# Kernel optimization log

Hardware: AMD Instinct MI355X
Metric: run time of the kernel (lower is better)

The kernel has to match this reference:

```python
import jax, jax.numpy as jnp
import numpy as np

B, H, W, C = 4, 48, 48, 768
L = H * W
D_STATE, D_CONV, D_INNER = 16, 4, C  # expand=1
DT_RANK = (C + 15) // 16  # 48


def generate_cross_scan_indices(Hh, Ww):
    indices = []
    visited = set()
    ch, cw = Hh // 2, Ww // 2
    indices.append((ch, cw)); visited.add((ch, cw))
    for radius in range(1, max(Hh, Ww)):
        for r in range(1, radius + 1):
            p = (ch - r, cw)
            if 0 <= p[0] < Hh and 0 <= p[1] < Ww and p not in visited: indices.append(p); visited.add(p)
        for r in range(1, radius + 1):
            p = (ch, cw + r)
            if 0 <= p[0] < Hh and 0 <= p[1] < Ww and p not in visited: indices.append(p); visited.add(p)
        for r in range(1, radius + 1):
            p = (ch + r, cw)
            if 0 <= p[0] < Hh and 0 <= p[1] < Ww and p not in visited: indices.append(p); visited.add(p)
        for r in range(1, radius + 1):
            p = (ch, cw - r)
            if 0 <= p[0] < Hh and 0 <= p[1] < Ww and p not in visited: indices.append(p); visited.add(p)
        for r in range(1, radius + 1):
            for p in [(ch - r, cw + r), (ch + r, cw + r), (ch + r, cw - r), (ch - r, cw - r)]:
                if 0 <= p[0] < Hh and 0 <= p[1] < Ww and p not in visited: indices.append(p); visited.add(p)
        for i in range(-radius, radius + 1):
            for j in range(-radius, radius + 1):
                p = (ch + i, cw + j)
                if 0 <= p[0] < Hh and 0 <= p[1] < Ww and p not in visited: indices.append(p); visited.add(p)
    return np.array([i * Ww + j for i, j in indices], dtype=np.int32)


def _mamba_params(key, scale=0.02):
    ks = jax.random.split(key, 6)
    return dict(
        in_w=jax.random.normal(ks[0], (2 * D_INNER, C)) * scale,
        conv_w=jax.random.normal(ks[1], (D_INNER, 1, D_CONV)) * scale,
        conv_b=jnp.zeros((D_INNER,)),
        xproj_w=jax.random.normal(ks[2], (DT_RANK + 2 * D_STATE, D_INNER)) * scale,
        dt_w=jax.random.normal(ks[3], (D_INNER, DT_RANK)) * scale,
        dt_b=jax.random.normal(ks[4], (D_INNER,)) * 0.1,
        A_log=jnp.broadcast_to(jnp.log(jnp.arange(1, D_STATE + 1, dtype=jnp.float32)), (D_INNER, D_STATE)).copy(),
        Dp=jnp.ones((D_INNER,)),
        out_w=jax.random.normal(ks[5], (C, D_INNER)) * scale,
    )


def setup_inputs() -> dict:
    key = jax.random.key(0)
    kx, kf, kb, k1, k2 = jax.random.split(key, 5)
    fp = _mamba_params(kf)
    bp = _mamba_params(kb)
    inp = {
        'x': jax.random.normal(kx, (B, L, C), dtype=jnp.float32),
        'scan_idx': jnp.asarray(generate_cross_scan_indices(H, W)),
        'norm_g': jnp.ones((C,)), 'norm_b': jnp.zeros((C,)),
        'fuse_w1': jax.random.normal(k1, (C, 2 * C)) * 0.02, 'fuse_b1': jnp.zeros((C,)),
        'fuse_w2': jax.random.normal(k2, (C, C)) * 0.02, 'fuse_b2': jnp.zeros((C,)),
    }
    for pre, p in (('f_', fp), ('b_', bp)):
        for n, v in p.items():
            inp[pre + n] = v
    return inp


def silu(v):
    return v * jax.nn.sigmoid(v)


def mamba(x, in_w, conv_w, conv_b, xproj_w, dt_w, dt_b, A_log, Dp, out_w):
    Bn, Ln, _ = x.shape
    xz = x @ in_w.T                      # [B,L,2*d_inner]
    xi, z = jnp.split(xz, 2, axis=-1)
    # causal depthwise conv1d, kernel D_CONV, left pad D_CONV-1
    xp = jnp.pad(xi, ((0, 0), (D_CONV - 1, 0), (0, 0)))
    xc = sum(conv_w[:, 0, k] * xp[:, k:k + Ln, :] for k in range(D_CONV)) + conv_b
    xc = silu(xc)                        # [B,L,d_inner]
    x_dbl = xc @ xproj_w.T
    dt, Bm, Cm = jnp.split(x_dbl, [DT_RANK, DT_RANK + D_STATE], axis=-1)
    dt = jax.nn.softplus(dt @ dt_w.T + dt_b)  # [B,L,d_inner]
    A = -jnp.exp(A_log)                  # [d_inner,d_state]

    def step(h, inps):
        dt_t, B_t, C_t, x_t = inps       # [B,d],[B,s],[B,s],[B,d]
        dA = jnp.exp(dt_t[:, :, None] * A)
        h = dA * h + (dt_t * x_t)[:, :, None] * B_t[:, None, :]
        y = jnp.einsum('bds,bs->bd', h, C_t)
        return h, y

    h0 = jnp.zeros((Bn, D_INNER, D_STATE), xc.dtype)
    xs = (dt.transpose(1, 0, 2), Bm.transpose(1, 0, 2), Cm.transpose(1, 0, 2), xc.transpose(1, 0, 2))
    _, ys = jax.lax.scan(step, h0, xs)
    y = ys.transpose(1, 0, 2) + Dp * xc
    y = y * silu(z)
    return y @ out_w.T


def reference(x, scan_idx, norm_g, norm_b, fuse_w1, fuse_b1, fuse_w2, fuse_b2,
              f_in_w, f_conv_w, f_conv_b, f_xproj_w, f_dt_w, f_dt_b, f_A_log, f_Dp, f_out_w,
              b_in_w, b_conv_w, b_conv_b, b_xproj_w, b_dt_w, b_dt_b, b_A_log, b_Dp, b_out_w):
    residual = x
    mu = x.mean(-1, keepdims=True)
    var = ((x - mu) ** 2).mean(-1, keepdims=True)
    xn = (x - mu) / jnp.sqrt(var + 1e-6) * norm_g + norm_b
    rev = jnp.argsort(scan_idx)
    xf = mamba(xn[:, scan_idx, :], f_in_w, f_conv_w, f_conv_b, f_xproj_w, f_dt_w, f_dt_b, f_A_log, f_Dp, f_out_w)[:, rev, :]
    flip = scan_idx[::-1]
    xb = mamba(xn[:, flip, :], b_in_w, b_conv_w, b_conv_b, b_xproj_w, b_dt_w, b_dt_b, b_A_log, b_Dp, b_out_w)[:, jnp.argsort(flip), :]
    fused = jnp.concatenate([xf, xb], axis=-1)
    h = jax.nn.gelu(fused @ fuse_w1.T + fuse_b1, approximate=False)
    out = h @ fuse_w2.T + fuse_b2
    return out + residual
```

## Files before the change

### kernel.cpp

```cpp
#include <hip/hip_runtime.h>
#include <hip/hip_bf16.h>
#include <cmath>

#define BB 4
#define LL 2304
#define CC 768
#define DSTATE 16
#define DINNER 768
#define DTRANK 48
#define MTOK (BB*LL)
#define NCH 48
#define LCH (LL/NCH)

#define S_XZ   14155776L
#define S_XC   7077888L
#define S_DT   7077888L
#define S_BC   294912L
#define S_YB   7077888L
#define S_AP   2359296L

#define L2E 1.4426950408889634f

typedef __bf16 bf16_t;
typedef __bf16 bf16x8 __attribute__((ext_vector_type(8)));
typedef float  f32x4  __attribute__((ext_vector_type(4)));

__device__ __forceinline__ float silu_f(float v){ return v / (1.0f + __expf(-v)); }
__device__ __forceinline__ float softplus_f(float v){
    return fmaxf(v,0.f) + __logf(1.0f + __expf(-fabsf(v)));
}

typedef __attribute__((address_space(3))) void  lds_vt;
typedef __attribute__((address_space(1))) void  gbl_vt;
__device__ __forceinline__ void async_copy16(const void* g, void* l){
    __builtin_amdgcn_global_load_lds((const gbl_vt*)g, (lds_vt*)l, 16, 0, 0);
}

__global__ __launch_bounds__(256)
void wconv_k(const float* __restrict__ a0, const float* __restrict__ a1,
             const float* __restrict__ a2, const float* __restrict__ a3,
             const float* __restrict__ a4, const float* __restrict__ a5,
             bf16_t* __restrict__ dst)
{
    const int cum[7]  = {0,1179648,2359296,3538944,4128768,4153344,4177920};
    const int dofs[6] = {0,1179648,2359296,3538944,4718592,5332992};
    const float* srcs[6] = {a0,a1,a2,a3,a4,a5};
    int idx = blockIdx.x*256 + threadIdx.x;
    if (idx >= 4177920) return;
    int seg = 0;
    while (idx >= cum[seg+1]) ++seg;
    dst[dofs[seg] + idx - cum[seg]] = (bf16_t)srcs[seg][idx - cum[seg]];
}

__global__ __launch_bounds__(256)
void transp_k(const float* __restrict__ s0, const float* __restrict__ s1,
              bf16_t* __restrict__ d0, bf16_t* __restrict__ d1)
{
    __shared__ float tile[32][33];
    const float* src = blockIdx.z ? s1 : s0;
    bf16_t* dst = blockIdx.z ? d1 : d0;
    int c0 = blockIdx.y*32, d0c = blockIdx.x*32;
    int tx = threadIdx.x & 31, ty = threadIdx.x >> 5;
#pragma unroll
    for (int r=0;r<4;++r)
        tile[ty+8*r][tx] = src[(long)(c0+ty+8*r)*768 + d0c+tx];
    __syncthreads();
#pragma unroll
    for (int r=0;r<4;++r)
        dst[(long)(d0c+ty+8*r)*768 + c0+tx] = (bf16_t)tile[tx][ty+8*r];
}

__global__ __launch_bounds__(256)
void inv_k(const int* __restrict__ sidx, int* __restrict__ rf, int* __restrict__ rb)
{
    int t = blockIdx.x*256 + threadIdx.x;
    if (t >= LL) return;
    rf[sidx[t]] = t;
    rb[sidx[LL-1-t]] = t;
}

__global__ __launch_bounds__(256)
void combo_k(const float* __restrict__ dtw, const float* __restrict__ xproj,
             bf16_t* __restrict__ dst)
{
    __shared__ float row[48];
    int n = blockIdx.x;
    if (threadIdx.x < 48) row[threadIdx.x] = dtw[n*48 + threadIdx.x];
    __syncthreads();
#pragma unroll
    for (int kk=0; kk<3; ++kk){
        int k = threadIdx.x + 256*kk;
        float s = 0.f;
#pragma unroll 8
        for (int r=0; r<48; ++r) s += row[r]*xproj[r*768 + k];
        dst[n*768 + k] = (bf16_t)s;
    }
}

__global__ __launch_bounds__(256)
void ln_k(const float* __restrict__ x, const float* __restrict__ g,
          const float* __restrict__ bta, bf16_t* __restrict__ xn)
{
    int row = blockIdx.x;
    const float* xr = x + (long)row*CC;
    int tid = threadIdx.x;
    float v[3];
#pragma unroll
    for (int r=0;r<3;++r) v[r] = xr[tid + 256*r];
    float s  = v[0]+v[1]+v[2];
    float s2 = v[0]*v[0]+v[1]*v[1]+v[2]*v[2];
    __shared__ float red[8];
    for (int o=32;o;o>>=1){ s += __shfl_down(s,o); s2 += __shfl_down(s2,o); }
    int wv = tid>>6, ln = tid&63;
    if (ln==0){ red[wv]=s; red[4+wv]=s2; }
    __syncthreads();
    if (tid==0){
        red[0] = red[0]+red[1]+red[2]+red[3];
        red[4] = red[4]+red[5]+red[6]+red[7];
    }
    __syncthreads();
    float mu  = red[0]*(1.0f/CC);
    float var = red[4]*(1.0f/CC) - mu*mu;
    float rstd = rsqrtf(var + 1e-6f);
#pragma unroll
    for (int r=0;r<3;++r){
        int c = tid + 256*r;
        xn[(long)row*CC + c] = (bf16_t)((v[r]-mu)*rstd*g[c] + bta[c]);
    }
}

#define CT 8
__global__ __launch_bounds__(256)
void conv_k(const bf16_t* __restrict__ xz, const float* __restrict__ cw0,
            const float* __restrict__ cw1, const float* __restrict__ cb0,
            const float* __restrict__ cb1, bf16_t* __restrict__ xc)
{
    int dir = blockIdx.y;
    const bf16_t* xzd = xz + (long)dir*S_XZ;
    const float* cw = dir ? cw1 : cw0;
    const float* cb = dir ? cb1 : cb0;
    bf16_t* xcd = xc + (long)dir*S_XC;
    int idx = blockIdx.x*256 + threadIdx.x;
    if (idx >= (MTOK/CT)*(DINNER/8)) return;
    int dg    = idx % (DINNER/8);
    int chunk = idx / (DINNER/8);
    int d0 = dg*8;
    long r0 = (long)chunk*CT;
    int t0 = (int)(r0 % LL);

    float4 wv[8];
#pragma unroll
    for (int u=0;u<8;++u) wv[u] = *(const float4*)&cw[(d0+u)*4];
    float bz[8];
#pragma unroll
    for (int u=0;u<8;++u) bz[u] = cb[d0+u];

    const bf16_t* src = xzd + r0*1536 + d0;
    bf16x8 win0, win1, win2;
    if (t0 >= 3){
        win0 = *(const bf16x8*)(src - 3*1536);
        win1 = *(const bf16x8*)(src - 2*1536);
        win2 = *(const bf16x8*)(src - 1*1536);
    } else {
#pragma unroll
        for (int u=0;u<8;++u){ win0[u]=(bf16_t)0.f; win1[u]=(bf16_t)0.f; win2[u]=(bf16_t)0.f; }
    }
#pragma unroll
    for (int t=0;t<CT;++t){
        bf16x8 cur = *(const bf16x8*)(src + (long)t*1536);
        bf16x8 o;
#pragma unroll
        for (int u=0;u<8;++u){
            float acc = bz[u]
                + wv[u].x*(float)win0[u] + wv[u].y*(float)win1[u]
                + wv[u].z*(float)win2[u] + wv[u].w*(float)cur[u];
            o[u] = (bf16_t)silu_f(acc);
        }
        *(bf16x8*)(xcd + (r0+t)*DINNER + d0) = o;
        win0 = win1; win1 = win2; win2 = cur;
    }
}

template<int GATHER, int SCATTER, int EPI>
__global__ __launch_bounds__(256)
void gemm4_k(const bf16_t* __restrict__ A, long a_stride, int lda,
             const bf16_t* __restrict__ W0, const bf16_t* __restrict__ W1,
             int N, int K,
             void* __restrict__ out1, long o1_stride,
             void* __restrict__ out2, long o2_stride,
             int ldc, int ccol_stride,
             const float* __restrict__ bias0, const float* __restrict__ bias1,
             const float* __restrict__ resid,
             const int* __restrict__ sidx,
             const int* __restrict__ ridx0, const int* __restrict__ ridx1)
{
    __shared__ __align__(16) bf16_t smem[2*128*64];
    bf16_t* As = smem;
    bf16_t* Bs = smem + 128*64;

    const int tid  = threadIdx.x;
    const int lane = tid & 63;
    const int w    = tid >> 6;
    const int ln16 = lane & 15;
    const int q    = lane >> 4;
    const int dir  = blockIdx.z;

    const bf16_t* Ad = A + (long)dir*a_stride;
    const bf16_t* W  = dir ? W1 : W0;
    const float* bias = dir ? bias1 : bias0;

    const int m0 = blockIdx.x*128;
    const int n0 = blockIdx.y*128;

    const int srow = lane >> 3;
    const int csrc = (lane & 7) ^ srow;
    const bf16_t* gA[4]; const bf16_t* gA1[4]; const bf16_t* gB[4];
#pragma unroll
    for (int inst=0; inst<4; ++inst){
        int row = w*32 + inst*8 + srow;
        int r = m0 + row;
        if (GATHER == 4){
            int t = r % LL; int bo = r - t;
            gA[inst]  = A + (long)(bo + ridx0[t])*lda + csrc*8;
            gA1[inst] = A + a_stride + (long)(bo + ridx1[t])*lda + csrc*8;
        } else {
            int sr = r;
            if (GATHER == 3){
                int t = r % LL; int bo = r - t;
                sr = bo + (dir ? sidx[LL-1-t] : sidx[t]);
            }
            gA[inst] = Ad + (long)sr*lda + csrc*8;
        }
        int n = n0 + row; if (n >= N) n = N-1;
        gB[inst] = W + (long)n*K + csrc*8;
    }

    f32x4 acc[4][4];
#pragma unroll
    for (int i=0;i<4;++i)
#pragma unroll
      for (int j=0;j<4;++j) acc[i][j] = (f32x4){0.f,0.f,0.f,0.f};

    const int e = ln16 & 7;
    const int ar_base = ((w>>1)*64 + ln16)*64;
    const int br_base = ((w&1)*64 + ln16)*64;

    for (int k0 = 0; k0 < K; k0 += 64){
#pragma unroll
        for (int inst=0; inst<4; ++inst){
            bf16_t* la = As + (w*256 + inst*64)*8;
            bf16_t* lb = Bs + (w*256 + inst*64)*8;
            const bf16_t* asrc;
            if (GATHER == 4)
                asrc = (k0 >= 768) ? (gA1[inst] + (k0 - 768)) : (gA[inst] + k0);
            else
                asrc = gA[inst] + k0;
            async_copy16(asrc, la);
            async_copy16(gB[inst] + k0, lb);
        }
        __syncthreads();
#pragma unroll
        for (int kk=0; kk<2; ++kk){
            const int ce = (((kk<<2)|q) ^ e)*8;
            bf16x8 af[4], bf[4];
#pragma unroll
            for (int i=0;i<4;++i) af[i] = *(const bf16x8*)&As[ar_base + i*16*64 + ce];
#pragma unroll
            for (int j=0;j<4;++j) bf[j] = *(const bf16x8*)&Bs[br_base + j*16*64 + ce];
#pragma unroll
            for (int i=0;i<4;++i)
#pragma unroll
              for (int j=0;j<4;++j)
                acc[i][j] = __builtin_amdgcn_mfma_f32_16x16x32_bf16(af[i], bf[j], acc[i][j], 0,0,0);
        }
        __syncthreads();
    }

    const int mw = (w>>1)*64;
    const int nw = (w&1)*64;
    const int ccolb = ccol_stride*dir;

    const bool staged = (EPI==2) || (EPI==3) || (EPI==5 && n0 < 768);
    if (staged){
        bf16_t* Cs = smem;
#pragma unroll
        for (int i=0;i<4;++i){
#pragma unroll
            for (int reg=0; reg<4; ++reg){
                int rowl = mw + i*16 + q*4 + reg;
#pragma unroll
                for (int j=0;j<4;++j){
                    int coll = nw + j*16 + ln16;
                    float v = acc[i][j][reg];
                    if (EPI==3){
                        v += bias[n0 + coll];
                        v = 0.5f*v*(1.0f + erff(v*0.70710678118654752f));
                    } else if (EPI==5){
                        v = softplus_f(v + bias[n0 + coll]);
                    }
                    Cs[rowl*128 + coll] = (bf16_t)v;
                }
            }
        }
        __syncthreads();
        bf16_t* o = (bf16_t*)out1 + (long)dir*o1_stride;
#pragma unroll
        for (int c=0;c<8;++c){
            int chunk = tid + 256*c;
            int rowl = chunk >> 4;
            int coll = (chunk & 15)*8;
            int r = m0 + rowl;
            int orow = r;
            if (SCATTER == 3){
                int t = r % LL; int bo = r - t;
                orow = bo + (dir ? sidx[LL-1-t] : sidx[t]);
            }
            *(int4*)&o[(long)orow*ldc + ccolb + n0 + coll] = *(const int4*)&Cs[rowl*128 + coll];
        }
    } else {
#pragma unroll
        for (int i=0;i<4;++i){
#pragma unroll
            for (int reg=0; reg<4; ++reg){
                int r = m0 + mw + i*16 + q*4 + reg;
#pragma unroll
                for (int j=0;j<4;++j){
                    int col = n0 + nw + j*16 + ln16;
                    if (col >= N) continue;
                    float v = acc[i][j][reg];
                    if (EPI==4){
                        v += bias[col] + resid[(long)r*CC + col];
                        ((float*)out1)[(long)r*ldc + col] = v;
                    } else {
                        ((float*)out2 + (long)dir*o2_stride)[(long)r*32 + (col-768)] = v;
                    }
                }
            }
        }
    }
}

template<int PASS>
__global__ __launch_bounds__(256)
void scanp_k(const bf16_t* __restrict__ dtp, const bf16_t* __restrict__ xcp,
             const float* __restrict__ bcp, const bf16_t* __restrict__ xzp,
             const float* __restrict__ Al0, const float* __restrict__ Al1,
             const float* __restrict__ Dp0, const float* __restrict__ Dp1,
             float* __restrict__ Aprod, float* __restrict__ Hend,
             bf16_t* __restrict__ yout)
{
    __shared__ __align__(16) float s_bc[LCH*32];

    const int dir = blockIdx.y;
    int blk = blockIdx.x;
    const int dblk = blk % 3; int tmp = blk / 3;
    const int j = tmp % NCH; const int b = tmp / NCH;
    const int tid = threadIdx.x;
    const long tbase = (long)b*LL + (long)j*LCH;
    const int d = dblk*256 + tid;

    const float* gbc = bcp + dir*S_BC + tbase*32;
    async_copy16(gbc + tid*4, s_bc + tid*4);
    if (tid < 128) async_copy16(gbc + (256+tid)*4, s_bc + (256+tid)*4);

    const float* Al = dir ? Al1 : Al0;
    float ac2[16]; bool fast = true;
#pragma unroll
    for (int k=0;k<16;++k){
        float a = -__expf(Al[d*DSTATE + k]);
        fast = fast && (fabsf(a + (float)(k+1)) < 1e-3f*(float)(k+1));
        ac2[k] = a * L2E;
    }

    __syncthreads();

    const bf16_t* gdt = dtp + dir*S_DT + tbase*DINNER + d;
    const bf16_t* gxc = xcp + dir*S_XC + tbase*DINNER + d;
    const bf16_t* gz  = xzp + dir*S_XZ + tbase*1536 + DINNER + d;
    bf16_t* gy = yout + dir*S_YB + tbase*DINNER + d;

    const long o = dir*S_AP + ((long)(b*NCH + j)*DINNER + d)*DSTATE;

    float h[16];
    float dpv = 0.f;
    if (PASS==3){
#pragma unroll
        for (int g=0; g<4; ++g){
            f32x4 hv = *(const f32x4*)&Aprod[o + 4*g];
#pragma unroll
            for (int k=0;k<4;++k) h[g*4+k] = hv[k];
        }
        dpv = (dir ? Dp1 : Dp0)[d];
    } else {
#pragma unroll
        for (int k=0;k<16;++k) h[k] = 0.f;
    }
    float sdt = 0.f;

#pragma unroll 2
    for (int t=0; t<LCH; ++t){
        float dt = (float)gdt[(long)t*DINNER];
        float xv = (float)gxc[(long)t*DINNER];
        float ek[16];
        if (fast){
            float e1 = __builtin_amdgcn_exp2f(-L2E*dt);
            ek[0]=e1;        ek[1]=e1*e1;      ek[2]=ek[1]*e1;   ek[3]=ek[1]*ek[1];
            ek[4]=ek[3]*e1;  ek[5]=ek[3]*ek[1];ek[6]=ek[3]*ek[2];ek[7]=ek[3]*ek[3];
            ek[8]=ek[7]*e1;  ek[9]=ek[7]*ek[1];ek[10]=ek[7]*ek[2];ek[11]=ek[7]*ek[3];
            ek[12]=ek[7]*ek[4];ek[13]=ek[7]*ek[5];ek[14]=ek[7]*ek[6];ek[15]=ek[7]*ek[7];
        } else {
#pragma unroll
            for (int k=0;k<16;++k) ek[k] = __builtin_amdgcn_exp2f(dt*ac2[k]);
        }
        float c = dt*xv;
        if (PASS==1) sdt += dt;
        const float* bcr = &s_bc[t*32];
#pragma unroll
        for (int g=0; g<4; ++g){
            f32x4 Bv = *(const f32x4*)&bcr[g*4];
#pragma unroll
            for (int k=0;k<4;++k) h[g*4+k] = ek[g*4+k]*h[g*4+k] + c*Bv[k];
        }
        if (PASS==3){
            f32x4 Cv0 = *(const f32x4*)&bcr[16];
            f32x4 Cv1 = *(const f32x4*)&bcr[20];
            f32x4 Cv2 = *(const f32x4*)&bcr[24];
            f32x4 Cv3 = *(const f32x4*)&bcr[28];
            float p0=0.f,p1=0.f,p2=0.f,p3=0.f;
#pragma unroll
            for (int k=0;k<4;++k){
                p0 += h[k]*Cv0[k];    p1 += h[4+k]*Cv1[k];
                p2 += h[8+k]*Cv2[k];  p3 += h[12+k]*Cv3[k];
            }
            float p = (p0+p1)+(p2+p3);
            float zv = (float)gz[(long)t*1536];
            gy[(long)t*DINNER] = (bf16_t)((p + dpv*xv) * silu_f(zv));
        }
    }

    if (PASS==1){
        float ap[16];
        if (fast){
            float e1 = __builtin_amdgcn_exp2f(-L2E*sdt);
            ap[0]=e1;        ap[1]=e1*e1;      ap[2]=ap[1]*e1;   ap[3]=ap[1]*ap[1];
            ap[4]=ap[3]*e1;  ap[5]=ap[3]*ap[1];ap[6]=ap[3]*ap[2];ap[7]=ap[3]*ap[3];
            ap[8]=ap[7]*e1;  ap[9]=ap[7]*ap[1];ap[10]=ap[7]*ap[2];ap[11]=ap[7]*ap[3];
            ap[12]=ap[7]*ap[4];ap[13]=ap[7]*ap[5];ap[14]=ap[7]*ap[6];ap[15]=ap[7]*ap[7];
        } else {
#pragma unroll
            for (int k=0;k<16;++k) ap[k] = __builtin_amdgcn_exp2f(sdt*ac2[k]);
        }
#pragma unroll
        for (int g=0; g<4; ++g){
            f32x4 av, hv;
#pragma unroll
            for (int k=0;k<4;++k){ av[k]=ap[g*4+k]; hv[k]=h[g*4+k]; }
            *(f32x4*)&Aprod[o+4*g] = av;
            *(f32x4*)&Hend[o+4*g]  = hv;
        }
    }
}

__global__ __launch_bounds__(256)
void scan2_k(float* __restrict__ Aprod, const float* __restrict__ Hend)
{
    int idx = blockIdx.x*256 + threadIdx.x;
    if (idx >= 2*BB*DINNER*DSTATE) return;
    int dir = idx / (BB*DINNER*DSTATE);
    int rem = idx - dir*(BB*DINNER*DSTATE);
    int b = rem / (DINNER*DSTATE);
    int ds = rem % (DINNER*DSTATE);
    long base = (long)dir*S_AP;
    float h = 0.f;
    for (int j=0;j<NCH;++j){
        long o = base + (long)(b*NCH+j)*DINNER*DSTATE + ds;
        float ap = Aprod[o];
        float he = Hend[o];
        Aprod[o] = h;
        h = ap*h + he;
    }
}

extern "C" void kernel_launch(void* const* d_in, const int* in_sizes, int n_in,
                              void* d_out, int out_size, void* d_ws, size_t ws_size,
                              hipStream_t stream)
{
    const float* x       = (const float*)d_in[0];
    const int*   sidx    = (const int*)  d_in[1];
    const float* norm_g  = (const float*)d_in[2];
    const float* norm_b  = (const float*)d_in[3];
    const float* fuse_w1 = (const float*)d_in[4];
    const float* fuse_b1 = (const float*)d_in[5];
    const float* fuse_w2 = (const float*)d_in[6];
    const float* fuse_b2 = (const float*)d_in[7];
    const float* f_in_w   = (const float*)d_in[8];
    const float* f_conv_w = (const float*)d_in[9];
    const float* f_conv_b = (const float*)d_in[10];
    const float* f_xproj  = (const float*)d_in[11];
    const float* f_dt_w   = (const float*)d_in[12];
    const float* f_dt_b   = (const float*)d_in[13];
    const float* f_A_log  = (const float*)d_in[14];
    const float* f_Dp     = (const float*)d_in[15];
    const float* f_out_w  = (const float*)d_in[16];
    const float* b_in_w   = (const float*)d_in[17];
    const float* b_conv_w = (const float*)d_in[18];
    const float* b_conv_b = (const float*)d_in[19];
    const float* b_xproj  = (const float*)d_in[20];
    const float* b_dt_w   = (const float*)d_in[21];
    const float* b_dt_b   = (const float*)d_in[22];
    const float* b_A_log  = (const float*)d_in[23];
    const float* b_Dp     = (const float*)d_in[24];
    const float* b_out_w  = (const float*)d_in[25];
    float* out = (float*)d_out;

    float* ws    = (float*)d_ws;
    bf16_t* xn   = (bf16_t*)ws;
    bf16_t* xz   = (bf16_t*)(ws + 3538944);
    bf16_t* xc   = (bf16_t*)(ws + 17694720);
    bf16_t* dtb  = (bf16_t*)(ws + 24772608);
    float* bc    = ws + 31850496;
    bf16_t* yb   = (bf16_t*)(ws + 32440320);
    bf16_t* h1   = (bf16_t*)(ws + 39518208);
    float* Aprod = ws + 43057152;
    float* Hend  = ws + 47775744;
    bf16_t* wbf  = (bf16_t*)(ws + 52494336);
    int* rev_f   = (int*)(ws + 56352768);
    int* rev_b   = rev_f + 2304;

    bf16_t* w_fin    = wbf + 0;
    bf16_t* w_bin    = wbf + 1179648;
    bf16_t* w_1      = wbf + 2359296;
    bf16_t* w_2      = wbf + 3538944;
    bf16_t* w_fcombo = wbf + 4128768;
    bf16_t* w_bcombo = wbf + 4743168;
    bf16_t* foutT    = wbf + 5357568;
    bf16_t* boutT    = wbf + 5947392;
    bf16_t* Ccat     = wbf + 6537216;

    wconv_k<<<16320, 256, 0, stream>>>(f_in_w, b_in_w, fuse_w1, fuse_w2,
                                       f_xproj + 48*768, b_xproj + 48*768, wbf);
    transp_k<<<dim3(24,24,2), 256, 0, stream>>>(f_out_w, b_out_w, foutT, boutT);
    inv_k<<<9, 256, 0, stream>>>(sidx, rev_f, rev_b);
    combo_k<<<768, 256, 0, stream>>>(f_dt_w, f_xproj, w_fcombo);
    combo_k<<<768, 256, 0, stream>>>(b_dt_w, b_xproj, w_bcombo);
    ln_k<<<MTOK, 256, 0, stream>>>(x, norm_g, norm_b, xn);
    gemm4_k<0,0,2><<<dim3(6,6,2), 256, 0, stream>>>(
        w_1, 768, 1536, foutT, boutT, 768, 768,
        Ccat, 0, nullptr, 0, 1536, 768, nullptr, nullptr, nullptr, nullptr,
        nullptr, nullptr);

    gemm4_k<3,0,2><<<dim3(72,12,2), 256, 0, stream>>>(
        xn, 0, CC, w_fin, w_bin, 1536, 768,
        xz, S_XZ, nullptr, 0, 1536, 0, nullptr, nullptr, nullptr, sidx,
        nullptr, nullptr);
    conv_k<<<dim3((MTOK/CT)*(DINNER/8)/256, 2), 256, 0, stream>>>(
        xz, f_conv_w, b_conv_w, f_conv_b, b_conv_b, xc);
    gemm4_k<0,0,5><<<dim3(72,7,2), 256, 0, stream>>>(
        xc, S_XC, DINNER, w_fcombo, w_bcombo, 800, 768,
        dtb, S_DT, bc, S_BC, 768, 0, f_dt_b, b_dt_b, nullptr, nullptr,
        nullptr, nullptr);
    scanp_k<1><<<dim3(BB*NCH*3,2), 256, 0, stream>>>(
        dtb, xc, bc, xz, f_A_log, b_A_log, f_Dp, b_Dp, Aprod, Hend, yb);
    scan2_k<<<384, 256, 0, stream>>>(Aprod, Hend);
    scanp_k<3><<<dim3(BB*NCH*3,2), 256, 0, stream>>>(
        dtb, xc, bc, xz, f_A_log, b_A_log, f_Dp, b_Dp, Aprod, Hend, yb);
    gemm4_k<4,0,3><<<dim3(72,6,1), 256, 0, stream>>>(
        yb, S_YB, DINNER, Ccat, Ccat, 768, 1536,
        h1, 0, nullptr, 0, 768, 0, fuse_b1, fuse_b1, nullptr, nullptr,
        rev_f, rev_b);
    gemm4_k<0,0,4><<<dim3(72,6,1), 256, 0, stream>>>(
        h1, 0, DINNER, w_2, w_2, 768, 768,
        out, 0, nullptr, 0, 768, 0, fuse_b2, fuse_b2, x, nullptr,
        nullptr, nullptr);
}
```

Measured before the change: 505.8 us.

## Store xz, xc and dt in time-packed layout for vectorized scan loads

The in-projection and dt/B/C GEMMs now write their outputs in a layout where 8 consecutive timesteps of each channel are contiguous. The scan kernel can then fetch dt, x and z as 16-byte vectors once every 8 steps instead of strided scalar loads every step. The conv kernel reads this packed layout and writes both a packed copy for the scan and a row-major copy for the next GEMM, reusing the xn and h1 buffers. The cost is extra transposing work in the GEMM epilogues and a second conv output write, plus reliance on those aliased buffers being free at that point.

```diff
diff --git a/kernel.cpp b/kernel.cpp
--- a/kernel.cpp
+++ b/kernel.cpp
@@ -18,6 +18,7 @@
 #define S_BC   294912L
 #define S_YB   7077888L
 #define S_AP   2359296L
+#define S_XCR  79036416L
 
 #define L2E 1.4426950408889634f
 
@@ -35,6 +36,7 @@
 __device__ __forceinline__ void async_copy16(const void* g, void* l){
     __builtin_amdgcn_global_load_lds((const gbl_vt*)g, (lds_vt*)l, 16, 0, 0);
 }
+
 
 __global__ __launch_bounds__(256)
 void wconv_k(const float* __restrict__ a0, const float* __restrict__ a1,
@@ -129,55 +131,53 @@
     }
 }
 
-#define CT 8
-__global__ __launch_bounds__(256)
-void conv_k(const bf16_t* __restrict__ xz, const float* __restrict__ cw0,
+__global__ __launch_bounds__(256)
+void conv_k(const bf16_t* __restrict__ xzT, const float* __restrict__ cw0,
             const float* __restrict__ cw1, const float* __restrict__ cb0,
-            const float* __restrict__ cb1, bf16_t* __restrict__ xc)
-{
-    int dir = blockIdx.y;
-    const bf16_t* xzd = xz + (long)dir*S_XZ;
+            const float* __restrict__ cb1, bf16_t* __restrict__ xcT,
+            bf16_t* __restrict__ xcR0, bf16_t* __restrict__ xcR1)
+{
+    const int dir = blockIdx.y;
+    const bf16_t* src = xzT + (long)dir*S_XZ;
+    bf16_t* dstT = xcT + (long)dir*S_XC;
+    bf16_t* dstR = dir ? xcR1 : xcR0;
     const float* cw = dir ? cw1 : cw0;
     const float* cb = dir ? cb1 : cb0;
-    bf16_t* xcd = xc + (long)dir*S_XC;
     int idx = blockIdx.x*256 + threadIdx.x;
-    if (idx >= (MTOK/CT)*(DINNER/8)) return;
-    int dg    = idx % (DINNER/8);
-    int chunk = idx / (DINNER/8);
-    int d0 = dg*8;
-    long r0 = (long)chunk*CT;
-    int t0 = (int)(r0 % LL);
-
-    float4 wv[8];
-#pragma unroll
-    for (int u=0;u<8;++u) wv[u] = *(const float4*)&cw[(d0+u)*4];
-    float bz[8];
-#pragma unroll
-    for (int u=0;u<8;++u) bz[u] = cb[d0+u];
-
-    const bf16_t* src = xzd + r0*1536 + d0;
-    bf16x8 win0, win1, win2;
-    if (t0 >= 3){
-        win0 = *(const bf16x8*)(src - 3*1536);
-        win1 = *(const bf16x8*)(src - 2*1536);
-        win2 = *(const bf16x8*)(src - 1*1536);
-    } else {
-#pragma unroll
-        for (int u=0;u<8;++u){ win0[u]=(bf16_t)0.f; win1[u]=(bf16_t)0.f; win2[u]=(bf16_t)0.f; }
-    }
-#pragma unroll
-    for (int t=0;t<CT;++t){
-        bf16x8 cur = *(const bf16x8*)(src + (long)t*1536);
-        bf16x8 o;
-#pragma unroll
-        for (int u=0;u<8;++u){
-            float acc = bz[u]
-                + wv[u].x*(float)win0[u] + wv[u].y*(float)win1[u]
-                + wv[u].z*(float)win2[u] + wv[u].w*(float)cur[u];
-            o[u] = (bf16_t)silu_f(acc);
-        }
-        *(bf16x8*)(xcd + (r0+t)*DINNER + d0) = o;
-        win0 = win1; win1 = win2; win2 = cur;
+    int d = idx % 768;
+    int chunk = idx / 768;
+    int tb = chunk*2;
+    int r0 = chunk*16;
+
+    bf16x8 c0 = *(const bf16x8*)&src[((long)tb*1536 + d)*8];
+    bf16x8 c1 = *(const bf16x8*)&src[((long)(tb+1)*1536 + d)*8];
+    float xm3, xm2, xm1;
+    if (r0 % LL){
+        bf16x8 pv = *(const bf16x8*)&src[((long)(tb-1)*1536 + d)*8];
+        xm3=(float)pv[5]; xm2=(float)pv[6]; xm1=(float)pv[7];
+    } else { xm3=0.f; xm2=0.f; xm1=0.f; }
+
+    float4 w = *(const float4*)&cw[d*4];
+    float bz = cb[d];
+
+    float xx[16];
+#pragma unroll
+    for (int u=0;u<8;++u){ xx[u]=(float)c0[u]; xx[8+u]=(float)c1[u]; }
+    bf16x8 o0, o1;
+#pragma unroll
+    for (int u=0;u<16;++u){
+        float cur = xx[u];
+        float acc = bz + w.x*xm3 + w.y*xm2 + w.z*xm1 + w.w*cur;
+        float r = silu_f(acc);
+        if (u < 8) o0[u] = (bf16_t)r; else o1[u-8] = (bf16_t)r;
+        xm3 = xm2; xm2 = xm1; xm1 = cur;
+    }
+    *(bf16x8*)&dstT[((long)tb*768 + d)*8]     = o0;
+    *(bf16x8*)&dstT[((long)(tb+1)*768 + d)*8] = o1;
+#pragma unroll
+    for (int u=0;u<8;++u){
+        dstR[(long)(r0+u)*DINNER + d]   = o0[u];
+        dstR[(long)(r0+8+u)*DINNER + d] = o1[u];
     }
 }
 
@@ -280,7 +280,8 @@
     const int nw = (w&1)*64;
     const int ccolb = ccol_stride*dir;
 
-    const bool staged = (EPI==2) || (EPI==3) || (EPI==5 && n0 < 768);
+    const bool staged = (EPI==2) || (EPI==3) || (EPI==6) ||
+                        ((EPI==5 || EPI==7) && n0 < 768);
     if (staged){
         bf16_t* Cs = smem;
 #pragma unroll
@@ -295,7 +296,7 @@
                     if (EPI==3){
                         v += bias[n0 + coll];
                         v = 0.5f*v*(1.0f + erff(v*0.70710678118654752f));
-                    } else if (EPI==5){
+                    } else if (EPI==5 || EPI==7){
                         v = softplus_f(v + bias[n0 + coll]);
                     }
                     Cs[rowl*128 + coll] = (bf16_t)v;
@@ -304,18 +305,32 @@
         }
         __syncthreads();
         bf16_t* o = (bf16_t*)out1 + (long)dir*o1_stride;
-#pragma unroll
-        for (int c=0;c<8;++c){
-            int chunk = tid + 256*c;
-            int rowl = chunk >> 4;
-            int coll = (chunk & 15)*8;
-            int r = m0 + rowl;
-            int orow = r;
-            if (SCATTER == 3){
-                int t = r % LL; int bo = r - t;
-                orow = bo + (dir ? sidx[LL-1-t] : sidx[t]);
-            }
-            *(int4*)&o[(long)orow*ldc + ccolb + n0 + coll] = *(const int4*)&Cs[rowl*128 + coll];
+        if (EPI==6 || EPI==7){
+#pragma unroll
+            for (int c=0;c<8;++c){
+                int chunk = tid + 256*c;
+                int nb  = chunk & 127;
+                int tbl = chunk >> 7;
+                bf16x8 v;
+#pragma unroll
+                for (int u=0;u<8;++u) v[u] = Cs[(tbl*8+u)*128 + nb];
+                long base = ((long)(m0/8 + tbl)*ldc + (n0 + nb))*8;
+                *(bf16x8*)&o[base] = v;
+            }
+        } else {
+#pragma unroll
+            for (int c=0;c<8;++c){
+                int chunk = tid + 256*c;
+                int rowl = chunk >> 4;
+                int coll = (chunk & 15)*8;
+                int r = m0 + rowl;
+                int orow = r;
+                if (SCATTER == 3){
+                    int t = r % LL; int bo = r - t;
+                    orow = bo + (dir ? sidx[LL-1-t] : sidx[t]);
+                }
+                *(int4*)&o[(long)orow*ldc + ccolb + n0 + coll] = *(const int4*)&Cs[rowl*128 + coll];
+            }
         }
     } else {
 #pragma unroll
@@ -357,6 +372,7 @@
     const int j = tmp % NCH; const int b = tmp / NCH;
     const int tid = threadIdx.x;
     const long tbase = (long)b*LL + (long)j*LCH;
+    const long tb0 = tbase >> 3;
     const int d = dblk*256 + tid;
 
     const float* gbc = bcp + dir*S_BC + tbase*32;
@@ -372,11 +388,9 @@
         ac2[k] = a * L2E;
     }
 
-    __syncthreads();
-
-    const bf16_t* gdt = dtp + dir*S_DT + tbase*DINNER + d;
-    const bf16_t* gxc = xcp + dir*S_XC + tbase*DINNER + d;
-    const bf16_t* gz  = xzp + dir*S_XZ + tbase*1536 + DINNER + d;
+    const bf16_t* gdt = dtp + dir*S_DT + (tb0*768  + d)*8;
+    const bf16_t* gxc = xcp + dir*S_XC + (tb0*768  + d)*8;
+    const bf16_t* gz  = xzp + dir*S_XZ + (tb0*1536 + 768 + d)*8;
     bf16_t* gy = yout + dir*S_YB + tbase*DINNER + d;
 
     const long o = dir*S_AP + ((long)(b*NCH + j)*DINNER + d)*DSTATE;
@@ -397,44 +411,54 @@
     }
     float sdt = 0.f;
 
+    __syncthreads();
+
 #pragma unroll 2
-    for (int t=0; t<LCH; ++t){
-        float dt = (float)gdt[(long)t*DINNER];
-        float xv = (float)gxc[(long)t*DINNER];
-        float ek[16];
-        if (fast){
-            float e1 = __builtin_amdgcn_exp2f(-L2E*dt);
-            ek[0]=e1;        ek[1]=e1*e1;      ek[2]=ek[1]*e1;   ek[3]=ek[1]*ek[1];
-            ek[4]=ek[3]*e1;  ek[5]=ek[3]*ek[1];ek[6]=ek[3]*ek[2];ek[7]=ek[3]*ek[3];
-            ek[8]=ek[7]*e1;  ek[9]=ek[7]*ek[1];ek[10]=ek[7]*ek[2];ek[11]=ek[7]*ek[3];
-            ek[12]=ek[7]*ek[4];ek[13]=ek[7]*ek[5];ek[14]=ek[7]*ek[6];ek[15]=ek[7]*ek[7];
-        } else {
-#pragma unroll
-            for (int k=0;k<16;++k) ek[k] = __builtin_amdgcn_exp2f(dt*ac2[k]);
-        }
-        float c = dt*xv;
-        if (PASS==1) sdt += dt;
-        const float* bcr = &s_bc[t*32];
-#pragma unroll
-        for (int g=0; g<4; ++g){
-            f32x4 Bv = *(const f32x4*)&bcr[g*4];
-#pragma unroll
-            for (int k=0;k<4;++k) h[g*4+k] = ek[g*4+k]*h[g*4+k] + c*Bv[k];
-        }
-        if (PASS==3){
-            f32x4 Cv0 = *(const f32x4*)&bcr[16];
-            f32x4 Cv1 = *(const f32x4*)&bcr[20];
-            f32x4 Cv2 = *(const f32x4*)&bcr[24];
-            f32x4 Cv3 = *(const f32x4*)&bcr[28];
-            float p0=0.f,p1=0.f,p2=0.f,p3=0.f;
-#pragma unroll
-            for (int k=0;k<4;++k){
-                p0 += h[k]*Cv0[k];    p1 += h[4+k]*Cv1[k];
-                p2 += h[8+k]*Cv2[k];  p3 += h[12+k]*Cv3[k];
-            }
-            float p = (p0+p1)+(p2+p3);
-            float zv = (float)gz[(long)t*1536];
-            gy[(long)t*DINNER] = (bf16_t)((p + dpv*xv) * silu_f(zv));
+    for (int cc=0; cc<LCH/8; ++cc){
+        bf16x8 vdt = *(const bf16x8*)&gdt[(long)cc*6144];
+        bf16x8 vxc = *(const bf16x8*)&gxc[(long)cc*6144];
+        bf16x8 vz;
+        if (PASS==3) vz = *(const bf16x8*)&gz[(long)cc*12288];
+#pragma unroll
+        for (int u=0; u<8; ++u){
+            const int t = cc*8 + u;
+            float dt = (float)vdt[u];
+            float xv = (float)vxc[u];
+            float ek[16];
+            if (fast){
+                float e1 = __builtin_amdgcn_exp2f(-L2E*dt);
+                ek[0]=e1;        ek[1]=e1*e1;      ek[2]=ek[1]*e1;   ek[3]=ek[1]*ek[1];
+                ek[4]=ek[3]*e1;  ek[5]=ek[3]*ek[1];ek[6]=ek[3]*ek[2];ek[7]=ek[3]*ek[3];
+                ek[8]=ek[7]*e1;  ek[9]=ek[7]*ek[1];ek[10]=ek[7]*ek[2];ek[11]=ek[7]*ek[3];
+                ek[12]=ek[7]*ek[4];ek[13]=ek[7]*ek[5];ek[14]=ek[7]*ek[6];ek[15]=ek[7]*ek[7];
+            } else {
+#pragma unroll
+                for (int k=0;k<16;++k) ek[k] = __builtin_amdgcn_exp2f(dt*ac2[k]);
+            }
+            float c = dt*xv;
+            if (PASS==1) sdt += dt;
+            const float* bcr = &s_bc[t*32];
+#pragma unroll
+            for (int g=0; g<4; ++g){
+                f32x4 Bv = *(const f32x4*)&bcr[g*4];
+#pragma unroll
+                for (int k=0;k<4;++k) h[g*4+k] = ek[g*4+k]*h[g*4+k] + c*Bv[k];
+            }
+            if (PASS==3){
+                f32x4 Cv0 = *(const f32x4*)&bcr[16];
+                f32x4 Cv1 = *(const f32x4*)&bcr[20];
+                f32x4 Cv2 = *(const f32x4*)&bcr[24];
+                f32x4 Cv3 = *(const f32x4*)&bcr[28];
+                float p0=0.f,p1=0.f,p2=0.f,p3=0.f;
+#pragma unroll
+                for (int k=0;k<4;++k){
+                    p0 += h[k]*Cv0[k];    p1 += h[4+k]*Cv1[k];
+                    p2 += h[8+k]*Cv2[k];  p3 += h[12+k]*Cv3[k];
+                }
+                float p = (p0+p1)+(p2+p3);
+                float zv = (float)vz[u];
+                gy[(long)t*DINNER] = (bf16_t)((p + dpv*xv) * silu_f(zv));
+            }
         }
     }
 
@@ -537,6 +561,9 @@
     bf16_t* boutT    = wbf + 5947392;
     bf16_t* Ccat     = wbf + 6537216;
 
+    bf16_t* xcR0 = xn;
+    bf16_t* xcR1 = h1;
+
     wconv_k<<<16320, 256, 0, stream>>>(f_in_w, b_in_w, fuse_w1, fuse_w2,
                                        f_xproj + 48*768, b_xproj + 48*768, wbf);
     transp_k<<<dim3(24,24,2), 256, 0, stream>>>(f_out_w, b_out_w, foutT, boutT);
@@ -549,14 +576,14 @@
         Ccat, 0, nullptr, 0, 1536, 768, nullptr, nullptr, nullptr, nullptr,
         nullptr, nullptr);
 
-    gemm4_k<3,0,2><<<dim3(72,12,2), 256, 0, stream>>>(
+    gemm4_k<3,0,6><<<dim3(72,12,2), 256, 0, stream>>>(
         xn, 0, CC, w_fin, w_bin, 1536, 768,
         xz, S_XZ, nullptr, 0, 1536, 0, nullptr, nullptr, nullptr, sidx,
         nullptr, nullptr);
-    conv_k<<<dim3((MTOK/CT)*(DINNER/8)/256, 2), 256, 0, stream>>>(
-        xz, f_conv_w, b_conv_w, f_conv_b, b_conv_b, xc);
-    gemm4_k<0,0,5><<<dim3(72,7,2), 256, 0, stream>>>(
-        xc, S_XC, DINNER, w_fcombo, w_bcombo, 800, 768,
+    conv_k<<<dim3(1728, 2), 256, 0, stream>>>(
+        xz, f_conv_w, b_conv_w, f_conv_b, b_conv_b, xc, xcR0, xcR1);
+    gemm4_k<0,0,7><<<dim3(72,7,2), 256, 0, stream>>>(
+        xcR0, S_XCR, DINNER, w_fcombo, w_bcombo, 800, 768,
         dtb, S_DT, bc, S_BC, 768, 0, f_dt_b, b_dt_b, nullptr, nullptr,
         nullptr, nullptr);
     scanp_k<1><<<dim3(BB*NCH*3,2), 256, 0, stream>>>(
```

Measured after the change: 594.4 us. 1.18x slower.
